# Kernel optimization log

Measured on AMD Instinct MI355X. Metric: run time of the kernel, lower is better.

Reference implementation:

```python
import jax, jax.numpy as jnp
import numpy as np


def setup_inputs() -> dict:
    key = jax.random.key(0)
    k1, k2, k3, k4 = jax.random.split(key, 4)
    B, D, F = 524288, 64, 32
    stdv = 1.0 / np.sqrt(D)
    x = jax.random.normal(k1, (B, D), dtype=jnp.float32)
    us = jax.random.uniform(k2, (F, D), dtype=jnp.float32, minval=-stdv, maxval=stdv)
    ws = jax.random.uniform(k3, (F, D), dtype=jnp.float32, minval=-stdv, maxval=stdv)
    bs = jax.random.uniform(k4, (F,), dtype=jnp.float32, minval=-0.01, maxval=0.01)
    return {"x": x, "us": us, "ws": ws, "bs": bs}


def _planar_step(carry, params):
    z, sum_log_det = carry
    u, w, b = params  # u,w: [D], b: scalar
    # constrained u for invertibility: u_hat = u + (softplus(wu) - 1 - wu) * w / ||w||
    wu = jnp.dot(u, w)
    u_hat = u + (jax.nn.softplus(wu) - 1.0 - wu) * w / jnp.linalg.norm(w)
    lin = z @ w + b                      # [B]
    h = jnp.tanh(lin)                    # [B]
    z_new = z + u_hat[None, :] * h[:, None]
    h_prime = 1.0 - h * h                # [B]
    # psi @ u_hat = h'(lin) * (w . u_hat)
    log_det = jnp.log(jnp.abs(1.0 + h_prime * jnp.dot(w, u_hat)))
    return (z_new, sum_log_det + log_det), None


def reference(x, us, ws, bs):
    init = (x, jnp.zeros(x.shape[0], dtype=x.dtype))
    (z, sum_log_det), _ = jax.lax.scan(_planar_step, init, (us, ws, bs))
    return z, sum_log_det
```

## Files before the change

### kernel.cpp

```cpp
#include <hip/hip_runtime.h>
#include <math.h>


#define NF_D 64
#define NF_F 32

typedef float f4 __attribute__((ext_vector_type(4)));
typedef float f32x4v __attribute__((ext_vector_type(4)));
typedef unsigned int u32;
typedef u32 u32x4 __attribute__((ext_vector_type(4)));
typedef short bf16x8 __attribute__((ext_vector_type(8)));

#define WS_WF   0
#define WS_UF   2048
#define WS_GT   3072
#define WS_WUH  4096
#define WS_TOT  4128

__device__ __forceinline__ u32 fbits(float x){ union{float f;u32 u;} c; c.f=x; return c.u; }
__device__ __forceinline__ float asf(u32 u){ union{u32 u;float f;} c; c.u=u; return c.f; }
__device__ __forceinline__ u32 bfrnd(float x){ u32 b=fbits(x); return (b + 0x7FFFu + ((b>>16)&1u)) >> 16; }
__device__ __forceinline__ bf16x8 asbf(u32x4 v){ union{u32x4 u; bf16x8 b;} c; c.u=v; return c.b; }

__global__ void nf_precompute(const float* __restrict__ us,
                              const float* __restrict__ ws,
                              u32* __restrict__ wsb) {
  __shared__ float s_u[NF_F][NF_D];
  float* wsf = (float*)wsb;
  int t = threadIdx.x;
  if (t < NF_F) {
    const float* u = us + t * NF_D;
    const float* w = ws + t * NF_D;
    float wu = 0.f, n2 = 0.f;
    for (int d = 0; d < NF_D; ++d) {
      wu = fmaf(u[d], w[d], wu);
      n2 = fmaf(w[d], w[d], n2);
    }
    float sp = fmaxf(wu, 0.f) + log1pf(expf(-fabsf(wu)));
    float coef = (sp - 1.f - wu) / sqrtf(n2);
    for (int d = 0; d < NF_D; ++d)
      s_u[t][d] = fmaf(coef, w[d], u[d]);
    wsf[WS_WUH + t] = fmaf(coef, n2, wu);
  }
  __syncthreads();
  for (int idx = t; idx < 8 * 64; idx += 256) {
    int lin = idx >> 6, l = idx & 63;
    int Mt = lin >> 2, Kt = (lin >> 1) & 1, p = lin & 1;
    int fm = 16 * Mt + (l & 15);
    int kb = 32 * Kt + 8 * (l >> 4);
    for (int i = 0; i < 4; ++i) {
      u32 pr[2];
      for (int e = 0; e < 2; ++e) {
        float w = ws[fm * NF_D + kb + 2 * i + e];
        u32 hb = fbits(w) & 0xFFFF0000u;
        pr[e] = (p == 0) ? (hb >> 16) : (fbits(w - asf(hb)) >> 16);
      }
      wsb[WS_WF + (lin * 64 + l) * 4 + i] = pr[0] | (pr[1] << 16);
    }
  }
  for (int idx = t; idx < 4 * 64; idx += 256) {
    int l = idx & 63;
    int d = 16 * (idx >> 6) + (l & 15);
    int fb = 8 * (l >> 4);
    for (int i = 0; i < 4; ++i) {
      u32 r0 = bfrnd(s_u[fb + 2 * i][d]);
      u32 r1 = bfrnd(s_u[fb + 2 * i + 1][d]);
      wsb[WS_UF + idx * 4 + i] = r0 | (r1 << 16);
    }
  }
  for (int i = t; i < NF_F * NF_F; i += 256) {
    int f = i >> 5, g = i & 31;
    float s = 0.f;
    if (g < f) {
      const float* w = ws + f * NF_D;
      for (int d = 0; d < NF_D; ++d) s = fmaf(s_u[g][d], w[d], s);
    }
    wsf[WS_GT + i] = s;
  }
}

__device__ __forceinline__ float fast_tanh(float x) {
  float e = __builtin_amdgcn_exp2f(x * 2.885390081777927f);
  return 1.f - 2.f * __builtin_amdgcn_rcpf(e + 1.f);
}

#define MFMA __builtin_amdgcn_mfma_f32_16x16x32_bf16

__global__ __launch_bounds__(256) void nf_main(
    const float* __restrict__ x,
    const float* __restrict__ bs,
    const u32* __restrict__ wsb,
    float* __restrict__ out_z,
    float* __restrict__ out_ld,
    int B) {
  __shared__ float S[4][64 * 33];
  __shared__ u32 H2[4][16 * 64];
  const float* wsf = (const float*)wsb;

  int wave = threadIdx.x >> 6;
  int l = threadIdx.x & 63;
  int ntiles = B / 64;
  int tile = blockIdx.x * 4 + wave;
  if (tile >= ntiles) tile = ntiles - 1;
  float* Sw = S[wave];
  u32* Hw = H2[wave];

  bf16x8 Wf[2][2][2], Uf[4];
  #pragma unroll
  for (int q = 0; q < 8; ++q)
    Wf[q >> 2][(q >> 1) & 1][q & 1] =
        asbf(*(const u32x4*)(wsb + WS_WF + (q * 64 + l) * 4));
  #pragma unroll
  for (int Nt = 0; Nt < 4; ++Nt)
    Uf[Nt] = asbf(*(const u32x4*)(wsb + WS_UF + (Nt * 64 + l) * 4));

  const float* xt = x + (size_t)tile * 64 * NF_D;

  f32x4v acc[2][4];
  #pragma unroll
  for (int Nt = 0; Nt < 4; ++Nt) {
    bf16x8 Xh[2], Xl[2];
    #pragma unroll
    for (int Kt = 0; Kt < 2; ++Kt) {
      const f4* xp = (const f4*)(xt + ((l & 15) + 16 * Nt) * NF_D +
                                 32 * Kt + 8 * (l >> 4));
      f4 xa = xp[0], xb = xp[1];
      float xs[8] = {xa.x, xa.y, xa.z, xa.w, xb.x, xb.y, xb.z, xb.w};
      u32x4 hw, lw;
      #pragma unroll
      for (int i = 0; i < 4; ++i) {
        u32 b0 = fbits(xs[2 * i]), b1 = fbits(xs[2 * i + 1]);
        u32 h0 = b0 & 0xFFFF0000u, h1 = b1 & 0xFFFF0000u;
        hw[i] = (h0 >> 16) | h1;
        lw[i] = (fbits(xs[2 * i] - asf(h0)) >> 16) |
                (fbits(xs[2 * i + 1] - asf(h1)) & 0xFFFF0000u);
      }
      Xh[Kt] = asbf(hw);
      Xl[Kt] = asbf(lw);
    }
    #pragma unroll
    for (int Mt = 0; Mt < 2; ++Mt) {
      f32x4v a = {0.f, 0.f, 0.f, 0.f};
      #pragma unroll
      for (int Kt = 0; Kt < 2; ++Kt) {
        a = MFMA(Wf[Mt][Kt][0], Xh[Kt], a, 0, 0, 0);
        a = MFMA(Wf[Mt][Kt][0], Xl[Kt], a, 0, 0, 0);
        a = MFMA(Wf[Mt][Kt][1], Xh[Kt], a, 0, 0, 0);
      }
      acc[Mt][Nt] = a;
    }
  }
  #pragma unroll
  for (int Mt = 0; Mt < 2; ++Mt)
    #pragma unroll
    for (int Nt = 0; Nt < 4; ++Nt)
      #pragma unroll
      for (int r = 0; r < 4; ++r)
        Sw[((l & 15) + 16 * Nt) * 33 + 16 * Mt + 4 * (l >> 4) + r] =
            acc[Mt][Nt][r];
  __syncthreads();

  const float* gt = wsf + WS_GT;
  const float* wuhp = wsf + WS_WUH;
  float h[NF_F];
  float ldp = 1.f;
  #pragma unroll
  for (int f = 0; f < NF_F; ++f) {
    float s = Sw[l * 33 + f] + bs[f];
    #pragma unroll
    for (int g = 0; g < f; ++g)
      s = fmaf(gt[f * 32 + g], h[g], s);
    float hf = fast_tanh(s);
    h[f] = hf;
    ldp *= fmaf(fmaf(-hf, hf, 1.f), wuhp[f], 1.f);
  }
  #pragma unroll
  for (int i = 0; i < 16; ++i)
    Hw[i * 64 + l] = (fbits(h[2 * i]) >> 16) | (fbits(h[2 * i + 1]) & 0xFFFF0000u);
  __syncthreads();

  float* zt = out_z + (size_t)tile * 64 * NF_D;
  #pragma unroll
  for (int Mt = 0; Mt < 4; ++Mt) {
    u32x4 hfw;
    #pragma unroll
    for (int i = 0; i < 4; ++i)
      hfw[i] = Hw[(4 * (l >> 4) + i) * 64 + (l & 15) + 16 * Mt];
    bf16x8 Hf = asbf(hfw);
    #pragma unroll
    for (int Nt = 0; Nt < 4; ++Nt) {
      f32x4v zz = {0.f, 0.f, 0.f, 0.f};
      zz = MFMA(Hf, Uf[Nt], zz, 0, 0, 0);
      #pragma unroll
      for (int r = 0; r < 4; ++r) {
        int brow = 16 * Mt + 4 * (l >> 4) + r;
        int d = (l & 15) + 16 * Nt;
        zt[brow * NF_D + d] = zz[r] + xt[brow * NF_D + d];
      }
    }
  }
  out_ld[(size_t)tile * 64 + l] =
      __builtin_amdgcn_logf(fabsf(ldp)) * 0.6931471805599453f;
}

extern "C" void kernel_launch(void* const* d_in, const int* in_sizes, int n_in,
                              void* d_out, int out_size, void* d_ws, size_t ws_size,
                              hipStream_t stream) {
  const float* x    = (const float*)d_in[0];
  const float* us   = (const float*)d_in[1];
  const float* ws_p = (const float*)d_in[2];
  const float* bs   = (const float*)d_in[3];
  const int B = in_sizes[0] / NF_D;

  u32* wsbuf = (u32*)d_ws;
  float* out = (float*)d_out;

  nf_precompute<<<1, 256, 0, stream>>>(us, ws_p, wsbuf);
  const int ntiles = B / 64;
  const int grid = (ntiles + 3) / 4;
  nf_main<<<grid, 256, 0, stream>>>(x, bs, wsbuf, out,
                                    out + (size_t)B * NF_D, B);
}
```

Measured before the change: 82.66 us.

## Stage z output through per-wave LDS for coalesced float4 stores, drop block syncs

Each wave now writes its MFMA output tiles into its own swizzled LDS slice and then stores z and reads the x residual as coalesced float4 rows, instead of scattered scalar global accesses. The separate H buffer is removed, so the S buffer is reused for the packed h values and LDS use goes down, which can allow more blocks per CU. Block-wide __syncthreads are replaced by wave barriers because each wave touches only its own slice. The triangular recurrence now uses f4 vectorised dot products over the G matrix. This adds ordering assumptions about LDS within a wave and some extra LDS traffic.

Result: slower. 90.78 us (+9.8%).

```diff
diff --git a/kernel.cpp b/kernel.cpp
--- a/kernel.cpp
+++ b/kernel.cpp
@@ -94,7 +94,6 @@
     float* __restrict__ out_ld,
     int B) {
   __shared__ float S[4][64 * 33];
-  __shared__ u32 H2[4][16 * 64];
   const float* wsf = (const float*)wsb;
 
   int wave = threadIdx.x >> 6;
@@ -103,7 +102,6 @@
   int tile = blockIdx.x * 4 + wave;
   if (tile >= ntiles) tile = ntiles - 1;
   float* Sw = S[wave];
-  u32* Hw = H2[wave];
 
   bf16x8 Wf[2][2][2], Uf[4];
   #pragma unroll
@@ -116,7 +114,6 @@
 
   const float* xt = x + (size_t)tile * 64 * NF_D;
 
-  f32x4v acc[2][4];
   #pragma unroll
   for (int Nt = 0; Nt < 4; ++Nt) {
     bf16x8 Xh[2], Xl[2];
@@ -147,57 +144,74 @@
         a = MFMA(Wf[Mt][Kt][0], Xl[Kt], a, 0, 0, 0);
         a = MFMA(Wf[Mt][Kt][1], Xh[Kt], a, 0, 0, 0);
       }
-      acc[Mt][Nt] = a;
-    }
-  }
-  #pragma unroll
-  for (int Mt = 0; Mt < 2; ++Mt)
-    #pragma unroll
-    for (int Nt = 0; Nt < 4; ++Nt)
       #pragma unroll
       for (int r = 0; r < 4; ++r)
-        Sw[((l & 15) + 16 * Nt) * 33 + 16 * Mt + 4 * (l >> 4) + r] =
-            acc[Mt][Nt][r];
-  __syncthreads();
+        Sw[((l & 15) + 16 * Nt) * 33 + 16 * Mt + 4 * (l >> 4) + r] = a[r];
+    }
+  }
 
   const float* gt = wsf + WS_GT;
   const float* wuhp = wsf + WS_WUH;
-  float h[NF_F];
+  f4 hq[8];
+  #pragma unroll
+  for (int q = 0; q < 8; ++q) hq[q] = (f4)(0.f);
   float ldp = 1.f;
   #pragma unroll
   for (int f = 0; f < NF_F; ++f) {
-    float s = Sw[l * 33 + f] + bs[f];
-    #pragma unroll
-    for (int g = 0; g < f; ++g)
-      s = fmaf(gt[f * 32 + g], h[g], s);
+    const f4* g4 = (const f4*)(gt + f * 32);
+    f4 a = (f4)(0.f);
+    #pragma unroll
+    for (int q = 0; q < (f + 3) / 4; ++q)
+      a += g4[q] * hq[q];
+    float s = Sw[l * 33 + f] + bs[f] + ((a.x + a.y) + (a.z + a.w));
     float hf = fast_tanh(s);
-    h[f] = hf;
     ldp *= fmaf(fmaf(-hf, hf, 1.f), wuhp[f], 1.f);
-  }
-  #pragma unroll
-  for (int i = 0; i < 16; ++i)
-    Hw[i * 64 + l] = (fbits(h[2 * i]) >> 16) | (fbits(h[2 * i + 1]) & 0xFFFF0000u);
-  __syncthreads();
+    hq[f >> 2][f & 3] = hf;
+  }
+  #pragma unroll
+  for (int i = 0; i < 16; ++i) {
+    u32 pk = (fbits(hq[i >> 1][(i & 1) * 2]) >> 16) |
+             (fbits(hq[i >> 1][(i & 1) * 2 + 1]) & 0xFFFF0000u);
+    Sw[i * 64 + l] = asf(pk);
+  }
+
+  bf16x8 Hf[4];
+  #pragma unroll
+  for (int Mt = 0; Mt < 4; ++Mt) {
+    u32x4 hw;
+    #pragma unroll
+    for (int i = 0; i < 4; ++i)
+      hw[i] = fbits(Sw[(4 * (l >> 4) + i) * 64 + (l & 15) + 16 * Mt]);
+    Hf[Mt] = asbf(hw);
+  }
 
   float* zt = out_z + (size_t)tile * 64 * NF_D;
   #pragma unroll
-  for (int Mt = 0; Mt < 4; ++Mt) {
-    u32x4 hfw;
-    #pragma unroll
-    for (int i = 0; i < 4; ++i)
-      hfw[i] = Hw[(4 * (l >> 4) + i) * 64 + (l & 15) + 16 * Mt];
-    bf16x8 Hf = asbf(hfw);
-    #pragma unroll
-    for (int Nt = 0; Nt < 4; ++Nt) {
-      f32x4v zz = {0.f, 0.f, 0.f, 0.f};
-      zz = MFMA(Hf, Uf[Nt], zz, 0, 0, 0);
-      #pragma unroll
-      for (int r = 0; r < 4; ++r) {
-        int brow = 16 * Mt + 4 * (l >> 4) + r;
-        int d = (l & 15) + 16 * Nt;
-        zt[brow * NF_D + d] = zz[r] + xt[brow * NF_D + d];
-      }
-    }
+  for (int p = 0; p < 2; ++p) {
+    #pragma unroll
+    for (int Mt = 0; Mt < 4; ++Mt) {
+      #pragma unroll
+      for (int nn = 0; nn < 2; ++nn) {
+        f32x4v zz = {0.f, 0.f, 0.f, 0.f};
+        zz = MFMA(Hf[Mt], Uf[2 * p + nn], zz, 0, 0, 0);
+        #pragma unroll
+        for (int r = 0; r < 4; ++r) {
+          int b = 16 * Mt + 4 * (l >> 4) + r;
+          int cs = ((l & 15) >> 2) + 4 * nn;
+          Sw[b * 32 + 4 * (cs ^ (b & 7)) + ((l & 15) & 3)] = zz[r];
+        }
+      }
+    }
+    __builtin_amdgcn_wave_barrier();
+    #pragma unroll
+    for (int i = 0; i < 8; ++i) {
+      int c = l + 64 * i;
+      int row = c >> 3, c4 = c & 7;
+      f4 zv = *(const f4*)(Sw + row * 32 + 4 * (c4 ^ (row & 7)));
+      f4 xv = *(const f4*)(xt + row * NF_D + 32 * p + 4 * c4);
+      *(f4*)(zt + row * NF_D + 32 * p + 4 * c4) = zv + xv;
+    }
+    __builtin_amdgcn_wave_barrier();
   }
   out_ld[(size_t)tile * 64 + l] =
       __builtin_amdgcn_logf(fabsf(ldp)) * 0.6931471805599453f;
```
